# Kernel tuning notes

Hardware: AMD Instinct MI355X
Metric: run time of the kernel (lower is better)

## Reference

```python
import jax, jax.numpy as jnp
import numpy as np
from jax import lax

BN_EPS = 1e-5
SQ_EPS = 1e-8


def squash(s, axis=-1):
    # v = (|s|^2 / (1+|s|^2)) * s / |s|
    n2 = jnp.sum(s * s, axis=axis, keepdims=True)
    return (n2 / (1.0 + n2)) * s / jnp.sqrt(n2 + SQ_EPS)


def setup_inputs() -> dict:
    key = jax.random.key(0)
    ks = jax.random.split(key, 5)
    B, C, H, W = 64, 512, 28, 28
    NUM_ROUTES = 8 * 10 * 10  # lower_num_caps * 10 * 10 after k9 s2 conv on 28x28
    features = jax.random.normal(ks[0], (B, C, H, W), jnp.float32)
    conv1_w = jax.random.normal(ks[1], (256, 512, 3, 3), jnp.float32) * 0.02
    conv1_b = jnp.zeros((256,), jnp.float32)
    bn_gamma = jnp.ones((256,), jnp.float32)
    bn_beta = jnp.zeros((256,), jnp.float32)
    bn_mean = jnp.zeros((256,), jnp.float32)
    bn_var = jnp.ones((256,), jnp.float32)
    prim_w = jax.random.normal(ks[2], (256, 256, 9, 9), jnp.float32) * 0.02
    prim_b = jnp.zeros((256,), jnp.float32)
    # routing transform: (num_routes, higher_num_caps, out_dim, in_dim)
    route_w = jax.random.normal(ks[3], (NUM_ROUTES, 2, 16, 32), jnp.float32) * 0.05
    return {"features": features, "conv1_w": conv1_w, "conv1_b": conv1_b,
            "bn_gamma": bn_gamma, "bn_beta": bn_beta, "bn_mean": bn_mean,
            "bn_var": bn_var, "prim_w": prim_w, "prim_b": prim_b,
            "route_w": route_w}


def reference(features, conv1_w, conv1_b, bn_gamma, bn_beta, bn_mean, bn_var,
              prim_w, prim_b, route_w):
    B = features.shape[0]
    dn = ("NCHW", "OIHW", "NCHW")
    # pre_conv: Conv2d(512->256, k3, pad1) + BatchNorm (eval) + ReLU
    x = lax.conv_general_dilated(features, conv1_w, (1, 1), "SAME",
                                 dimension_numbers=dn)
    x = x + conv1_b[None, :, None, None]
    inv = bn_gamma * lax.rsqrt(bn_var + BN_EPS)
    x = x * inv[None, :, None, None] + (bn_beta - bn_mean * inv)[None, :, None, None]
    x = jax.nn.relu(x)
    # primary capsules: Conv2d(256->8*32, k9, s2, valid) -> (B,256,10,10)
    p = lax.conv_general_dilated(x, prim_w, (2, 2), "VALID",
                                 dimension_numbers=dn)
    p = p + prim_b[None, :, None, None]
    Hp, Wp = p.shape[2], p.shape[3]
    # (B, num_caps, cap_dim, Hp*Wp) -> (B, num_caps*Hp*Wp, cap_dim)
    p = p.reshape(B, 8, 32, Hp * Wp).transpose(0, 1, 3, 2).reshape(B, 8 * Hp * Wp, 32)
    lower_caps = squash(p, axis=-1)  # (B, 800, 32)
    # predictions u_hat: (B, routes, higher_caps, out_dim)
    u_hat = jnp.einsum("bri,rjoi->brjo", lower_caps, route_w)
    # dynamic routing-by-agreement
    b = jnp.zeros((B, u_hat.shape[1], u_hat.shape[2]), u_hat.dtype)
    n_iter = 3
    for it in range(n_iter):
        c = jax.nn.softmax(b, axis=2)                  # coupling coeffs
        s = jnp.einsum("brj,brjo->bjo", c, u_hat)      # weighted sum
        v = squash(s, axis=-1)                          # (B, 2, 16)
        if it < n_iter - 1:
            b = b + jnp.einsum("brjo,bjo->brj", u_hat, v)
    return (lower_caps, v)
```

## Files before the change

### kernel.cpp

```cpp
#include <hip/hip_runtime.h>
#include <hip/hip_bf16.h>

#define BN_EPS 1e-5f
#define SQ_EPS 1e-8f

typedef __hip_bfloat16 bf16;
typedef __attribute__((ext_vector_type(8))) short bf16x8;
typedef __attribute__((ext_vector_type(4))) float f32x4;

__device__ __forceinline__ void gload_lds16(const void* g, void* l) {
    __builtin_amdgcn_global_load_lds(
        (const __attribute__((address_space(1))) unsigned int*)g,
        (__attribute__((address_space(3))) unsigned int*)l, 16, 0, 0);
}

__device__ __forceinline__ unsigned short f2bfu(float f) {
    bf16 h = __float2bfloat16(f);
    return *(unsigned short*)&h;
}

__global__ __launch_bounds__(256) void feat_to_nhwc(
    const float* __restrict__ feat, bf16* __restrict__ featP) {
    int b = blockIdx.z, ct = blockIdx.y, pt = blockIdx.x;
    int ci0 = ct * 64, px0 = pt * 64;
    int tid = threadIdx.x;
    __shared__ float t[64][65];
#pragma unroll
    for (int rep = 0; rep < 16; rep++) {
        int ci_l = rep * 4 + (tid >> 6);
        int px = px0 + (tid & 63);
        float v = 0.f;
        if (px < 784) v = feat[(b * 512 + ci0 + ci_l) * 784 + px];
        t[ci_l][tid & 63] = v;
    }
    __syncthreads();
#pragma unroll
    for (int rep = 0; rep < 4; rep++) {
        int px_l = rep * 16 + (tid >> 4);
        int px = px0 + px_l;
        if (px < 784) {
            int h = px / 28, wq = px % 28;
            int ci = (tid & 15) * 4;
            ushort4 o;
            o.x = f2bfu(t[ci + 0][px_l]);
            o.y = f2bfu(t[ci + 1][px_l]);
            o.z = f2bfu(t[ci + 2][px_l]);
            o.w = f2bfu(t[ci + 3][px_l]);
            *(ushort4*)&featP[((b * 30 + h + 1) * 30 + (wq + 1)) * 512 + ci0 + ci] = o;
        }
    }
}

__global__ __launch_bounds__(256) void zero_ring(bf16* __restrict__ featP) {
    int b = blockIdx.x;
    uint4 zz = {0u, 0u, 0u, 0u};
    for (int i = threadIdx.x; i < 116 * 64; i += 256) {
        int rp = i >> 6;
        int ci = (i & 63) * 8;
        int hp, wp;
        if (rp < 30)      { hp = 0;       wp = rp; }
        else if (rp < 60) { hp = 29;      wp = rp - 30; }
        else if (rp < 88) { hp = rp - 59; wp = 0; }
        else              { hp = rp - 87; wp = 29; }
        *(uint4*)&featP[(b * 900 + hp * 30 + wp) * 512 + ci] = zz;
    }
}

__global__ __launch_bounds__(256) void w1F_transform(
    const float* __restrict__ w, bf16* __restrict__ wt1F) {
    int co = blockIdx.x;
    __shared__ float t1[4608];
    const float* src = w + co * 4608;
    for (int i = threadIdx.x; i < 4608; i += 256) t1[i] = src[i];
    __syncthreads();
    int co16 = co >> 4, l15 = co & 15;
    for (int i = threadIdx.x; i < 576; i += 256) {
        int g = i >> 6, cc = (i >> 2) & 15, kq = i & 3;
        short v[8];
#pragma unroll
        for (int j = 0; j < 8; j++) {
            unsigned short u = f2bfu(t1[(cc * 32 + kq * 8 + j) * 9 + g]);
            v[j] = (short)u;
        }
        int fidx = g * 16 + cc;
        bf16x8* dst = (bf16x8*)&wt1F[(fidx * 16 + co16) * 512 + (kq * 16 + l15) * 8];
        bf16x8 pk = {v[0], v[1], v[2], v[3], v[4], v[5], v[6], v[7]};
        *dst = pk;
    }
}

__global__ __launch_bounds__(256) void w2F_transform(
    const float* __restrict__ w, bf16* __restrict__ wt2F) {
    int half = blockIdx.x, co = blockIdx.y;
    __shared__ float t2[10368];
    const float* src = w + co * 20736 + half * 10368;
    for (int i = threadIdx.x; i < 10368; i += 256) t2[i] = src[i];
    __syncthreads();
    int co16 = co >> 4, l15 = co & 15;
    for (int i = threadIdx.x; i < 1296; i += 256) {
        int sh = i >> 4, ccl = (i >> 2) & 3, kq = i & 3;
        int z = sh / 10; if (z > 7) z = 7;
        int s0 = (81 * z) >> 3;
        int fidx = s0 * 8 + (sh - s0) * 8 + (half * 4 + ccl);
        short v[8];
#pragma unroll
        for (int j = 0; j < 8; j++) {
            unsigned short u = f2bfu(t2[(ccl * 32 + kq * 8 + j) * 81 + sh]);
            v[j] = (short)u;
        }
        bf16x8* dst = (bf16x8*)&wt2F[(fidx * 16 + co16) * 512 + (kq * 16 + l15) * 8];
        bf16x8 pk = {v[0], v[1], v[2], v[3], v[4], v[5], v[6], v[7]};
        *dst = pk;
    }
}

__global__ __launch_bounds__(256, 2) void conv1_mfma(
    const bf16* __restrict__ featP, const bf16* __restrict__ wt1F,
    const float* __restrict__ bias, const float* __restrict__ gamma,
    const float* __restrict__ beta, const float* __restrict__ mean,
    const float* __restrict__ var, bf16* __restrict__ x) {
    __shared__ char As4[4 * 8192];
    const int tid = threadIdx.x, lane = tid & 63, w = tid >> 6;
    const int Mt = blockIdx.x;

    const bf16 *pA0, *pA1;
    {
        int r0 = (w << 5) + (lane >> 2);
        int r0c = r0 < 112 ? r0 : 111;
        int q0 = (lane & 3) ^ ((r0c >> 1) & 3);
        int m0 = Mt * 112 + r0c;
        int b0 = m0 / 784, rr = m0 % 784, h0 = rr / 28, w0 = rr % 28;
        pA0 = featP + ((b0 * 30 + h0) * 30 + w0) * 512 + q0 * 8;
        int r1 = r0 + 16;
        int r1c = r1 < 112 ? r1 : 111;
        int q1 = (lane & 3) ^ ((r1c >> 1) & 3);
        int m1 = Mt * 112 + r1c;
        int b1 = m1 / 784, rr1 = m1 % 784, h1 = rr1 / 28, w1 = rr1 % 28;
        pA1 = featP + ((b1 * 30 + h1) * 30 + w1) * 512 + q1 * 8;
    }
    const bf16x8* pB = (const bf16x8*)wt1F + w * 256 + lane;

    int a_off[7];
#pragma unroll
    for (int mi = 0; mi < 7; mi++) {
        int r = mi * 16 + (lane & 15);
        a_off[mi] = r * 64 + (((lane >> 4) ^ ((r >> 1) & 3)) * 16);
    }

    f32x4 acc[7][4];
#pragma unroll
    for (int i = 0; i < 7; i++)
#pragma unroll
        for (int j = 0; j < 4; j++) acc[i][j] = f32x4{0.f, 0.f, 0.f, 0.f};

    bf16x8 Bv0[4], Bv1[4];

#define STG1(bi, offE)                                                     \
    do {                                                                   \
        gload_lds16(pA0 + (offE), As4 + (bi) * 8192 + w * 2048);           \
        gload_lds16(pA1 + (offE), As4 + (bi) * 8192 + w * 2048 + 1024);    \
    } while (0)

    STG1(0, 0); STG1(1, 32); STG1(2, 64);
    { const bf16x8* bp = pB;
      Bv0[0] = bp[0]; Bv0[1] = bp[64]; Bv0[2] = bp[128]; Bv0[3] = bp[192]; }
    asm volatile("s_waitcnt vmcnt(8)" ::: "memory");
    __builtin_amdgcn_s_barrier();
    asm volatile("" ::: "memory");

#define C1_STEP(u, BU, BL)                                                 \
    do {                                                                   \
        const int t_ = t + (u);                                            \
        const int tt = t_ + 3;                                             \
        {       \
            int g_ = tt >> 4; if (g_ > 8) g_ = 8;                          \
            int cc_ = tt & 15;                                             \
            int ky_ = g_ / 3, kx_ = g_ - 3 * ky_;                          \
            STG1((u + 3) & 3, ky_ * 15360 + kx_ * 512 + cc_ * 32);         \
        }                                                                  \
        {                                                                  \
            int fn = t_ + 1; if (fn > 143) fn = 143;                       \
            const bf16x8* bp = pB + fn * 1024;                             \
            BL[0] = bp[0]; BL[1] = bp[64];                                 \
            BL[2] = bp[128]; BL[3] = bp[192];                              \
        }                                                                  \
        const char* Ab = As4 + (u) * 8192;                                 \
        bf16x8 af[7];                                                      \
        _Pragma("unroll")                                                  \
        for (int mi = 0; mi < 7; mi++)                                     \
            af[mi] = *(const bf16x8*)(Ab + a_off[mi]);                     \
        __builtin_amdgcn_s_setprio(1);                                     \
        _Pragma("unroll")                                                  \
        for (int nj = 0; nj < 4; nj++)                                     \
            _Pragma("unroll")                                              \
            for (int mi = 0; mi < 7; mi++)                                 \
                acc[mi][nj] = __builtin_amdgcn_mfma_f32_16x16x32_bf16(     \
                    af[mi], BU[nj], acc[mi][nj], 0, 0, 0);                 \
        __builtin_amdgcn_s_setprio(0);                                     \
        if (t_ < 143) {                                                    \
            asm volatile("s_waitcnt vmcnt(16)" ::: "memory");              \
            __builtin_amdgcn_s_barrier();                                  \
            asm volatile("" ::: "memory");                                 \
        }                                                                  \
    } while (0)

    for (int t = 0; t < 144; t += 4) {
        C1_STEP(0, Bv0, Bv1);
        C1_STEP(1, Bv1, Bv0);
        C1_STEP(2, Bv0, Bv1);
        C1_STEP(3, Bv1, Bv0);
    }

#pragma unroll
    for (int nj = 0; nj < 4; nj++) {
        int co = w * 64 + nj * 16 + (lane & 15);
        float inv = gamma[co] * rsqrtf(var[co] + BN_EPS);
        float sh = beta[co] - mean[co] * inv;
        float bs = bias[co];
#pragma unroll
        for (int mi = 0; mi < 7; mi++) {
            int m0 = Mt * 112 + mi * 16 + ((lane >> 4) << 2);
#pragma unroll
            for (int r = 0; r < 4; r++) {
                float v = (acc[mi][nj][r] + bs) * inv + sh;
                x[(m0 + r) * 256 + co] = __float2bfloat16(fmaxf(v, 0.f));
            }
        }
    }
#undef STG1
#undef C1_STEP
}

__global__ __launch_bounds__(256, 2) void conv2_mfma(
    const bf16* __restrict__ x, const bf16* __restrict__ wt2F,
    bf16* __restrict__ p_parts) {
    __shared__ char As4[4 * 8192];
    const int tid = threadIdx.x, lane = tid & 63, w = tid >> 6;
    const int z = blockIdx.x & 7, Mt = blockIdx.x >> 3;
    const int sh0 = (81 * z) >> 3, sh1 = (81 * (z + 1)) >> 3;
    const int NT = (sh1 - sh0) << 3;
    const int FB = sh0 << 3;

    const bf16 *pA0, *pA1;
    {
        int r0 = (w << 5) + (lane >> 2);
        int q0 = (lane & 3) ^ ((r0 >> 1) & 3);
        int m0 = Mt * 128 + r0;
        int b0 = m0 / 100, s0 = m0 % 100, ho0 = s0 / 10, wo0 = s0 % 10;
        pA0 = x + ((b0 * 28 + 2 * ho0) * 28 + 2 * wo0) * 256 + q0 * 8;
        int r1 = r0 + 16;
        int q1 = (lane & 3) ^ ((r1 >> 1) & 3);
        int m1 = Mt * 128 + r1;
        int b1 = m1 / 100, s1 = m1 % 100, ho1 = s1 / 10, wo1 = s1 % 10;
        pA1 = x + ((b1 * 28 + 2 * ho1) * 28 + 2 * wo1) * 256 + q1 * 8;
    }
    const bf16x8* pB = (const bf16x8*)wt2F + w * 256 + lane;

    int a_off[8];
#pragma unroll
    for (int mi = 0; mi < 8; mi++) {
        int r = mi * 16 + (lane & 15);
        a_off[mi] = r * 64 + (((lane >> 4) ^ ((r >> 1) & 3)) * 16);
    }

    f32x4 acc[8][4];
#pragma unroll
    for (int i = 0; i < 8; i++)
#pragma unroll
        for (int j = 0; j < 4; j++) acc[i][j] = f32x4{0.f, 0.f, 0.f, 0.f};

    bf16x8 Bv0[4], Bv1[4];

#define STG2(bi, offE)                                                     \
    do {                                                                   \
        gload_lds16(pA0 + (offE), As4 + (bi) * 8192 + w * 2048);           \
        gload_lds16(pA1 + (offE), As4 + (bi) * 8192 + w * 2048 + 1024);    \
    } while (0)

#define A2OFF(tt)                                                          \
    ({ int sh_ = sh0 + ((tt) >> 3); if (sh_ > 80) sh_ = 80;                \
       int cc_ = (tt) & 7;                                                 \
       int ky_ = sh_ / 9, kx_ = sh_ - 9 * ky_;                             \
       (ky_ * 28 + kx_) * 256 + cc_ * 32; })

    STG2(0, A2OFF(0)); STG2(1, A2OFF(1)); STG2(2, A2OFF(2));
    { const bf16x8* bp = pB + FB * 1024;
      Bv0[0] = bp[0]; Bv0[1] = bp[64]; Bv0[2] = bp[128]; Bv0[3] = bp[192]; }
    asm volatile("s_waitcnt vmcnt(8)" ::: "memory");
    __builtin_amdgcn_s_barrier();
    asm volatile("" ::: "memory");

#define C2_STEP(u, BU, BL)                                                 \
    do {                                                                   \
        const int t_ = t + (u);                                            \
        const int tt = t_ + 3;                                             \
        STG2((u + 3) & 3, A2OFF(tt));                                      \
        {                                                                  \
            int fn = t_ + 1; if (fn > NT - 1) fn = NT - 1;                 \
            const bf16x8* bp = pB + (FB + fn) * 1024;                      \
            BL[0] = bp[0]; BL[1] = bp[64];                                 \
            BL[2] = bp[128]; BL[3] = bp[192];                              \
        }                                                                  \
        const char* Ab = As4 + (u) * 8192;                                 \
        bf16x8 af[8];                                                      \
        _Pragma("unroll")                                                  \
        for (int mi = 0; mi < 8; mi++)                                     \
            af[mi] = *(const bf16x8*)(Ab + a_off[mi]);                     \
        __builtin_amdgcn_s_setprio(1);                                     \
        _Pragma("unroll")                                                  \
        for (int nj = 0; nj < 4; nj++)                                     \
            _Pragma("unroll")                                              \
            for (int mi = 0; mi < 8; mi++)                                 \
                acc[mi][nj] = __builtin_amdgcn_mfma_f32_16x16x32_bf16(     \
                    af[mi], BU[nj], acc[mi][nj], 0, 0, 0);                 \
        __builtin_amdgcn_s_setprio(0);                                     \
        if (t_ < NT - 1) {                                                 \
            asm volatile("s_waitcnt vmcnt(16)" ::: "memory");              \
            __builtin_amdgcn_s_barrier();                                  \
            asm volatile("" ::: "memory");                                 \
        }                                                                  \
    } while (0)

    for (int t = 0; t < NT; t += 4) {
        C2_STEP(0, Bv0, Bv1);
        C2_STEP(1, Bv1, Bv0);
        C2_STEP(2, Bv0, Bv1);
        C2_STEP(3, Bv1, Bv0);
    }

#pragma unroll
    for (int nj = 0; nj < 4; nj++) {
        int co = w * 64 + nj * 16 + (lane & 15);
#pragma unroll
        for (int mi = 0; mi < 8; mi++) {
            int m0 = Mt * 128 + mi * 16 + ((lane >> 4) << 2);
#pragma unroll
            for (int r = 0; r < 4; r++)
                p_parts[(z * 6400 + m0 + r) * 256 + co] =
                    __float2bfloat16(acc[mi][nj][r]);
        }
    }
#undef STG2
#undef A2OFF
#undef C2_STEP
}

__global__ __launch_bounds__(256) void squash_kernel(
    const bf16* __restrict__ pp, const float* __restrict__ pb,
    float* __restrict__ lc) {
    int rowg = blockIdx.x * 8 + (threadIdx.x >> 5);
    int i = threadIdx.x & 31;
    int b = rowg / 800, r = rowg - b * 800;
    int cap = r / 100, s = r - cap * 100;
    int m = b * 100 + s, co = cap * 32 + i;
    float val = pb[co];
#pragma unroll
    for (int zz = 0; zz < 8; zz++)
        val += __bfloat162float(pp[(zz * 6400 + m) * 256 + co]);
    float n2 = val * val;
#pragma unroll
    for (int msk = 1; msk < 32; msk <<= 1) n2 += __shfl_xor(n2, msk);
    float scale = n2 / ((1.f + n2) * sqrtf(n2 + SQ_EPS));
    lc[(b * 800 + r) * 32 + i] = val * scale;
}

__global__ __launch_bounds__(256) void uhat_kernel(
    const float* __restrict__ lc, const float* __restrict__ rw,
    bf16* __restrict__ uht) {
    int rT = blockIdx.x, bT = blockIdx.y;
    int rl = threadIdx.x >> 5, jo = threadIdx.x & 31;
    int r = rT * 8 + rl;
    float4 wreg[8];
    const float4* wp4 = reinterpret_cast<const float4*>(rw + (r * 32 + jo) * 32);
#pragma unroll
    for (int k = 0; k < 8; k++) wreg[k] = wp4[k];
    for (int b = bT * 16; b < bT * 16 + 16; b++) {
        const float4* lp4 = reinterpret_cast<const float4*>(lc + (b * 800 + r) * 32);
        float acc = 0.f;
#pragma unroll
        for (int k = 0; k < 8; k++) {
            float4 a = lp4[k];
            acc = fmaf(a.x, wreg[k].x, acc);
            acc = fmaf(a.y, wreg[k].y, acc);
            acc = fmaf(a.z, wreg[k].z, acc);
            acc = fmaf(a.w, wreg[k].w, acc);
        }
        uht[(b * 32 + jo) * 800 + r] = __float2bfloat16(acc);
    }
}

__global__ __launch_bounds__(256) void route_all(
    const bf16* __restrict__ uht, float* __restrict__ vout) {
    extern __shared__ float rs[];
    float* u = rs;
    float* lg = rs + 26400;
    float* red = lg + 1600;
    float* vs = red + 256;
    int b = blockIdx.x, tid = threadIdx.x;
    for (int i = tid; i < 25600; i += 256) {
        int jo = i / 800, r = i - jo * 800;
        u[r * 33 + jo] = __bfloat162float(uht[(b * 32 + jo) * 800 + r]);
    }
    for (int i = tid; i < 1600; i += 256) lg[i] = 0.f;
    __syncthreads();
    int jo = tid & 31, rg = tid >> 5;
    for (int it = 0; it < 3; it++) {
        float sp = 0.f;
        for (int r = rg; r < 800; r += 8) {
            float l0 = lg[r * 2], l1 = lg[r * 2 + 1];
            float m = fmaxf(l0, l1);
            float e0 = __expf(l0 - m), e1 = __expf(l1 - m);
            float c = ((jo < 16) ? e0 : e1) / (e0 + e1);
            sp += c * u[r * 33 + jo];
        }
        red[rg * 32 + jo] = sp;
        __syncthreads();
        if (tid < 32) {
            float s = 0.f;
#pragma unroll
            for (int k = 0; k < 8; k++) s += red[k * 32 + tid];
            float n2 = s * s;
#pragma unroll
            for (int m = 1; m < 16; m <<= 1) n2 += __shfl_xor(n2, m);
            float scale = n2 / ((1.f + n2) * sqrtf(n2 + SQ_EPS));
            float v = s * scale;
            vs[tid] = v;
            if (it == 2) vout[b * 32 + tid] = v;
        }
        __syncthreads();
        if (it < 2) {
            for (int r = tid; r < 800; r += 256) {
                float d0 = 0.f, d1 = 0.f;
#pragma unroll
                for (int o = 0; o < 16; o++) {
                    d0 += u[r * 33 + o] * vs[o];
                    d1 += u[r * 33 + 16 + o] * vs[16 + o];
                }
                lg[r * 2] += d0;
                lg[r * 2 + 1] += d1;
            }
            __syncthreads();
        }
    }
}

extern "C" void kernel_launch(void* const* d_in, const int* in_sizes, int n_in,
                              void* d_out, int out_size, void* d_ws, size_t ws_size,
                              hipStream_t stream) {
    const float* feat    = (const float*)d_in[0];
    const float* conv1_w = (const float*)d_in[1];
    const float* conv1_b = (const float*)d_in[2];
    const float* bn_g    = (const float*)d_in[3];
    const float* bn_b    = (const float*)d_in[4];
    const float* bn_m    = (const float*)d_in[5];
    const float* bn_v    = (const float*)d_in[6];
    const float* prim_w  = (const float*)d_in[7];
    const float* prim_b  = (const float*)d_in[8];
    const float* route_w = (const float*)d_in[9];
    float* out = (float*)d_out;

    char* wsb = (char*)d_ws;
    bf16*  featP   = (bf16*)(wsb + 0);
    bf16*  p_parts = (bf16*)(wsb + 0);
    bf16*  uht     = (bf16*)(wsb + 26214400);
    bf16*  x       = (bf16*)(wsb + 58982400);
    bf16*  wt1F    = (bf16*)(wsb + 84672512);
    bf16*  wt2F    = (bf16*)(wsb + 87031808);

    float* lc_out = out;
    float* v_out  = out + 64 * 800 * 32;

    hipFuncSetAttribute((const void*)route_all,
                        hipFuncAttributeMaxDynamicSharedMemorySize, 113152);

    feat_to_nhwc<<<dim3(13, 8, 64), 256, 0, stream>>>(feat, featP);
    zero_ring<<<64, 256, 0, stream>>>(featP);
    w1F_transform<<<256, 256, 0, stream>>>(conv1_w, wt1F);
    w2F_transform<<<dim3(2, 256), 256, 0, stream>>>(prim_w, wt2F);

    conv1_mfma<<<448, 256, 0, stream>>>(
        featP, wt1F, conv1_b, bn_g, bn_b, bn_m, bn_v, x);

    conv2_mfma<<<400, 256, 0, stream>>>(x, wt2F, p_parts);

    squash_kernel<<<6400, 256, 0, stream>>>(p_parts, prim_b, lc_out);

    uhat_kernel<<<dim3(100, 4), 256, 0, stream>>>(lc_out, route_w, uht);

    route_all<<<64, 256, 113152, stream>>>(uht, v_out);
}
```

Baseline: 318.1 us.

## Split conv1 across 8 waves, reorder K loop by position, merge weight transforms

conv1 now runs 512 threads per block with eight waves, each owning 32 output channels instead of 64. This halves the per-wave accumulators and B registers so more waves fit per CU. The K loop order changes so consecutive steps advance over spatial taps within a channel chunk rather than over channel chunks, with matching weight layout changes for both convs. The two weight-transform kernels are merged into one launch. The trade-off is that each staged A tile is reused by fewer MFMAs per wave, and there are more barrier participants and a different global access pattern for A.

```diff
diff --git a/kernel.cpp b/kernel.cpp
--- a/kernel.cpp
+++ b/kernel.cpp
@@ -66,79 +66,73 @@
     }
 }
 
-__global__ __launch_bounds__(256) void w1F_transform(
-    const float* __restrict__ w, bf16* __restrict__ wt1F) {
-    int co = blockIdx.x;
-    __shared__ float t1[4608];
-    const float* src = w + co * 4608;
-    for (int i = threadIdx.x; i < 4608; i += 256) t1[i] = src[i];
-    __syncthreads();
-    int co16 = co >> 4, l15 = co & 15;
-    for (int i = threadIdx.x; i < 576; i += 256) {
-        int g = i >> 6, cc = (i >> 2) & 15, kq = i & 3;
-        short v[8];
-#pragma unroll
-        for (int j = 0; j < 8; j++) {
-            unsigned short u = f2bfu(t1[(cc * 32 + kq * 8 + j) * 9 + g]);
-            v[j] = (short)u;
-        }
-        int fidx = g * 16 + cc;
-        bf16x8* dst = (bf16x8*)&wt1F[(fidx * 16 + co16) * 512 + (kq * 16 + l15) * 8];
-        bf16x8 pk = {v[0], v[1], v[2], v[3], v[4], v[5], v[6], v[7]};
-        *dst = pk;
-    }
-}
-
-__global__ __launch_bounds__(256) void w2F_transform(
-    const float* __restrict__ w, bf16* __restrict__ wt2F) {
-    int half = blockIdx.x, co = blockIdx.y;
-    __shared__ float t2[10368];
-    const float* src = w + co * 20736 + half * 10368;
-    for (int i = threadIdx.x; i < 10368; i += 256) t2[i] = src[i];
-    __syncthreads();
-    int co16 = co >> 4, l15 = co & 15;
-    for (int i = threadIdx.x; i < 1296; i += 256) {
-        int sh = i >> 4, ccl = (i >> 2) & 3, kq = i & 3;
-        int z = sh / 10; if (z > 7) z = 7;
-        int s0 = (81 * z) >> 3;
-        int fidx = s0 * 8 + (sh - s0) * 8 + (half * 4 + ccl);
-        short v[8];
-#pragma unroll
-        for (int j = 0; j < 8; j++) {
-            unsigned short u = f2bfu(t2[(ccl * 32 + kq * 8 + j) * 81 + sh]);
-            v[j] = (short)u;
-        }
-        bf16x8* dst = (bf16x8*)&wt2F[(fidx * 16 + co16) * 512 + (kq * 16 + l15) * 8];
-        bf16x8 pk = {v[0], v[1], v[2], v[3], v[4], v[5], v[6], v[7]};
-        *dst = pk;
-    }
-}
-
-__global__ __launch_bounds__(256, 2) void conv1_mfma(
+__global__ __launch_bounds__(256) void wF_transform(
+    const float* __restrict__ w1, const float* __restrict__ w2,
+    bf16* __restrict__ wt1F, bf16* __restrict__ wt2F) {
+    __shared__ float tt[10368];
+    if (blockIdx.x < 256) {
+        int co = blockIdx.x;
+        const float* src = w1 + co * 4608;
+        for (int i = threadIdx.x; i < 4608; i += 256) tt[i] = src[i];
+        __syncthreads();
+        int co16 = co >> 4, l15 = co & 15;
+        for (int i = threadIdx.x; i < 576; i += 256) {
+            int g = i >> 6, cc = (i >> 2) & 15, kq = i & 3;
+            short v[8];
+#pragma unroll
+            for (int j = 0; j < 8; j++) {
+                unsigned short u = f2bfu(tt[(cc * 32 + kq * 8 + j) * 9 + g]);
+                v[j] = (short)u;
+            }
+            int fidx = cc * 9 + g;
+            bf16x8* dst = (bf16x8*)&wt1F[(fidx * 16 + co16) * 512 + (kq * 16 + l15) * 8];
+            bf16x8 pk = {v[0], v[1], v[2], v[3], v[4], v[5], v[6], v[7]};
+            *dst = pk;
+        }
+    } else {
+        int bid = blockIdx.x - 256;
+        int half = bid & 1, co = bid >> 1;
+        const float* src = w2 + co * 20736 + half * 10368;
+        for (int i = threadIdx.x; i < 10368; i += 256) tt[i] = src[i];
+        __syncthreads();
+        int co16 = co >> 4, l15 = co & 15;
+        for (int i = threadIdx.x; i < 1296; i += 256) {
+            int sh = i >> 4, ccl = (i >> 2) & 3, kq = i & 3;
+            int z = sh / 10; if (z > 7) z = 7;
+            int s0 = (81 * z) >> 3;
+            int ns = ((81 * (z + 1)) >> 3) - s0;
+            int fidx = s0 * 8 + (half * 4 + ccl) * ns + (sh - s0);
+            short v[8];
+#pragma unroll
+            for (int j = 0; j < 8; j++) {
+                unsigned short u = f2bfu(tt[(ccl * 32 + kq * 8 + j) * 81 + sh]);
+                v[j] = (short)u;
+            }
+            bf16x8* dst = (bf16x8*)&wt2F[(fidx * 16 + co16) * 512 + (kq * 16 + l15) * 8];
+            bf16x8 pk = {v[0], v[1], v[2], v[3], v[4], v[5], v[6], v[7]};
+            *dst = pk;
+        }
+    }
+}
+
+__global__ __launch_bounds__(512, 4) void conv1_mfma(
     const bf16* __restrict__ featP, const bf16* __restrict__ wt1F,
     const float* __restrict__ bias, const float* __restrict__ gamma,
     const float* __restrict__ beta, const float* __restrict__ mean,
     const float* __restrict__ var, bf16* __restrict__ x) {
-    __shared__ char As4[4 * 8192];
+    __shared__ char As4[4 * 7168];
     const int tid = threadIdx.x, lane = tid & 63, w = tid >> 6;
     const int Mt = blockIdx.x;
 
-    const bf16 *pA0, *pA1;
+    const bf16* pA0;
     {
-        int r0 = (w << 5) + (lane >> 2);
-        int r0c = r0 < 112 ? r0 : 111;
-        int q0 = (lane & 3) ^ ((r0c >> 1) & 3);
-        int m0 = Mt * 112 + r0c;
+        int r0 = (w << 4) + (lane >> 2);
+        int q = (lane & 3) ^ ((r0 >> 1) & 3);
+        int m0 = Mt * 112 + (w < 7 ? r0 : 0);
         int b0 = m0 / 784, rr = m0 % 784, h0 = rr / 28, w0 = rr % 28;
-        pA0 = featP + ((b0 * 30 + h0) * 30 + w0) * 512 + q0 * 8;
-        int r1 = r0 + 16;
-        int r1c = r1 < 112 ? r1 : 111;
-        int q1 = (lane & 3) ^ ((r1c >> 1) & 3);
-        int m1 = Mt * 112 + r1c;
-        int b1 = m1 / 784, rr1 = m1 % 784, h1 = rr1 / 28, w1 = rr1 % 28;
-        pA1 = featP + ((b1 * 30 + h1) * 30 + w1) * 512 + q1 * 8;
-    }
-    const bf16x8* pB = (const bf16x8*)wt1F + w * 256 + lane;
+        pA0 = featP + ((b0 * 30 + h0) * 30 + w0) * 512 + q * 8;
+    }
+    const bf16x8* pB = (const bf16x8*)wt1F + w * 128 + lane;
 
     int a_off[7];
 #pragma unroll
@@ -147,58 +141,55 @@
         a_off[mi] = r * 64 + (((lane >> 4) ^ ((r >> 1) & 3)) * 16);
     }
 
-    f32x4 acc[7][4];
+    f32x4 acc[7][2];
 #pragma unroll
     for (int i = 0; i < 7; i++)
 #pragma unroll
-        for (int j = 0; j < 4; j++) acc[i][j] = f32x4{0.f, 0.f, 0.f, 0.f};
-
-    bf16x8 Bv0[4], Bv1[4];
+        for (int j = 0; j < 2; j++) acc[i][j] = f32x4{0.f, 0.f, 0.f, 0.f};
+
+    bf16x8 Bv0[2], Bv1[2];
 
 #define STG1(bi, offE)                                                     \
     do {                                                                   \
-        gload_lds16(pA0 + (offE), As4 + (bi) * 8192 + w * 2048);           \
-        gload_lds16(pA1 + (offE), As4 + (bi) * 8192 + w * 2048 + 1024);    \
+        if (w < 7)                                                         \
+            gload_lds16(pA0 + (offE), As4 + (bi) * 7168 + w * 1024);       \
     } while (0)
 
-    STG1(0, 0); STG1(1, 32); STG1(2, 64);
-    { const bf16x8* bp = pB;
-      Bv0[0] = bp[0]; Bv0[1] = bp[64]; Bv0[2] = bp[128]; Bv0[3] = bp[192]; }
-    asm volatile("s_waitcnt vmcnt(8)" ::: "memory");
+    STG1(0, 0); STG1(1, 512); STG1(2, 1024);
+    { const bf16x8* bp = pB; Bv0[0] = bp[0]; Bv0[1] = bp[64]; }
+    asm volatile("s_waitcnt vmcnt(2)" ::: "memory");
     __builtin_amdgcn_s_barrier();
     asm volatile("" ::: "memory");
 
 #define C1_STEP(u, BU, BL)                                                 \
     do {                                                                   \
         const int t_ = t + (u);                                            \
-        const int tt = t_ + 3;                                             \
+        int ttc = t_ + 3; if (ttc > 143) ttc = 143;                        \
         {       \
-            int g_ = tt >> 4; if (g_ > 8) g_ = 8;                          \
-            int cc_ = tt & 15;                                             \
+            int cc_ = ttc / 9, g_ = ttc - 9 * cc_;                         \
             int ky_ = g_ / 3, kx_ = g_ - 3 * ky_;                          \
-            STG1((u + 3) & 3, ky_ * 15360 + kx_ * 512 + cc_ * 32);         \
+            STG1((u + 3) & 3, (ky_ * 30 + kx_) * 512 + cc_ * 32);          \
         }                                                                  \
         {                                                                  \
             int fn = t_ + 1; if (fn > 143) fn = 143;                       \
             const bf16x8* bp = pB + fn * 1024;                             \
             BL[0] = bp[0]; BL[1] = bp[64];                                 \
-            BL[2] = bp[128]; BL[3] = bp[192];                              \
         }                                                                  \
-        const char* Ab = As4 + (u) * 8192;                                 \
+        const char* Ab = As4 + (u) * 7168;                                 \
         bf16x8 af[7];                                                      \
         _Pragma("unroll")                                                  \
         for (int mi = 0; mi < 7; mi++)                                     \
             af[mi] = *(const bf16x8*)(Ab + a_off[mi]);                     \
         __builtin_amdgcn_s_setprio(1);                                     \
         _Pragma("unroll")                                                  \
-        for (int nj = 0; nj < 4; nj++)                                     \
+        for (int nj = 0; nj < 2; nj++)                                     \
             _Pragma("unroll")                                              \
             for (int mi = 0; mi < 7; mi++)                                 \
                 acc[mi][nj] = __builtin_amdgcn_mfma_f32_16x16x32_bf16(     \
                     af[mi], BU[nj], acc[mi][nj], 0, 0, 0);                 \
         __builtin_amdgcn_s_setprio(0);                                     \
         if (t_ < 143) {                                                    \
-            asm volatile("s_waitcnt vmcnt(16)" ::: "memory");              \
+            asm volatile("s_waitcnt vmcnt(8)" ::: "memory");               \
             __builtin_amdgcn_s_barrier();                                  \
             asm volatile("" ::: "memory");                                 \
         }                                                                  \
@@ -212,8 +203,8 @@
     }
 
 #pragma unroll
-    for (int nj = 0; nj < 4; nj++) {
-        int co = w * 64 + nj * 16 + (lane & 15);
+    for (int nj = 0; nj < 2; nj++) {
+        int co = w * 32 + nj * 16 + (lane & 15);
         float inv = gamma[co] * rsqrtf(var[co] + BN_EPS);
         float sh = beta[co] - mean[co] * inv;
         float bs = bias[co];
@@ -238,7 +229,8 @@
     const int tid = threadIdx.x, lane = tid & 63, w = tid >> 6;
     const int z = blockIdx.x & 7, Mt = blockIdx.x >> 3;
     const int sh0 = (81 * z) >> 3, sh1 = (81 * (z + 1)) >> 3;
-    const int NT = (sh1 - sh0) << 3;
+    const int nsh = sh1 - sh0;
+    const int NT = nsh << 3;
     const int FB = sh0 << 3;
 
     const bf16 *pA0, *pA1;
@@ -278,8 +270,9 @@
     } while (0)
 
 #define A2OFF(tt)                                                          \
-    ({ int sh_ = sh0 + ((tt) >> 3); if (sh_ > 80) sh_ = 80;                \
-       int cc_ = (tt) & 7;                                                 \
+    ({ int ttc_ = (tt) < NT ? (tt) : NT - 1;                               \
+       int cc_ = ttc_ / nsh, si_ = ttc_ - cc_ * nsh;                       \
+       int sh_ = sh0 + si_;                                                \
        int ky_ = sh_ / 9, kx_ = sh_ - 9 * ky_;                             \
        (ky_ * 28 + kx_) * 256 + cc_ * 32; })
 
@@ -293,8 +286,7 @@
 #define C2_STEP(u, BU, BL)                                                 \
     do {                                                                   \
         const int t_ = t + (u);                                            \
-        const int tt = t_ + 3;                                             \
-        STG2((u + 3) & 3, A2OFF(tt));                                      \
+        STG2((u + 3) & 3, A2OFF(t_ + 3));                                  \
         {                                                                  \
             int fn = t_ + 1; if (fn > NT - 1) fn = NT - 1;                 \
             const bf16x8* bp = pB + (FB + fn) * 1024;                      \
@@ -475,10 +467,9 @@
 
     feat_to_nhwc<<<dim3(13, 8, 64), 256, 0, stream>>>(feat, featP);
     zero_ring<<<64, 256, 0, stream>>>(featP);
-    w1F_transform<<<256, 256, 0, stream>>>(conv1_w, wt1F);
-    w2F_transform<<<dim3(2, 256), 256, 0, stream>>>(prim_w, wt2F);
-
-    conv1_mfma<<<448, 256, 0, stream>>>(
+    wF_transform<<<768, 256, 0, stream>>>(conv1_w, prim_w, wt1F, wt2F);
+
+    conv1_mfma<<<448, 512, 0, stream>>>(
         featP, wt1F, conv1_b, bn_g, bn_b, bn_m, bn_v, x);
 
     conv2_mfma<<<400, 256, 0, stream>>>(x, wt2F, p_parts);
```

Measured after the change: 307.0 us. 1.04x faster.
